# Optimization experiments

Measured on AMD Instinct MI355X. Metric: run time of the kernel, lower is better.

## Reference

```python
import jax, jax.numpy as jnp
import numpy as np

B, C, S, H = 64, 64, 128, 512   # batch, num_centroid, max_seq_length, hidden_size
D = S * H
EPS = 1e-8


def setup_inputs() -> dict:
    key = jax.random.key(0)
    k1, k2 = jax.random.split(key)
    return {
        "input": jax.random.normal(k1, (B, D), dtype=jnp.float32),
        "centroid_weight": jax.random.normal(k2, (C, D), dtype=jnp.float32),
    }


def _gram(x):
    # x: (..., S, H) -> (..., S, S)
    return jnp.einsum('...sh,...th->...st', x, x)


def _centering(g):
    # H @ g @ H with H = I - 11^T/n  ==  g - rowmean - colmean + grandmean
    rm = jnp.mean(g, axis=-1, keepdims=True)
    cm = jnp.mean(g, axis=-2, keepdims=True)
    gm = jnp.mean(g, axis=(-1, -2), keepdims=True)
    return g - rm - cm + gm


def reference(input, centroid_weight):
    # torch.cdist(input, centroid_weight), p=2
    x2 = jnp.sum(input * input, axis=1, keepdims=True)        # (B,1)
    w2 = jnp.sum(centroid_weight * centroid_weight, axis=1)   # (C,)
    d2 = x2 + w2[None, :] - 2.0 * (input @ centroid_weight.T)
    dist = jnp.sqrt(jnp.maximum(d2, 0.0))                     # (B,C)

    xb = input.reshape(B, S, H)
    cw = centroid_weight.reshape(C, S, H)

    cgx = _centering(_gram(xb))   # (B,S,S)
    cgy = _centering(_gram(cw))   # (C,S,S)

    # linear HSIC(x,y) summed over last two dims, broadcast (B,1)x(C) -> (B,C)
    hxy = jnp.einsum('bst,cst->bc', cgx, cgy)
    hxx = jnp.sum(cgx * cgx, axis=(-1, -2))   # (B,)
    hyy = jnp.sum(cgy * cgy, axis=(-1, -2))   # (C,)
    cka_mat = -jnp.log(
        jnp.abs(hxy / (jnp.sqrt(hxx)[:, None] * jnp.sqrt(hyy)[None, :])) + EPS
    )  # (B,C)

    idx = jnp.argmax(cka_mat, axis=-1)                 # (B,)
    sel = centroid_weight[idx].reshape(B, S, H)        # selected centroids
    cgs = _centering(_gram(sel))                       # (B,S,S)

    # second CKA: x is (B,1,S,S), y is (B,S,S) -> broadcast to (B,B) as in torch
    hxy2 = jnp.einsum('bst,cst->bc', cgx, cgs)         # (B,B)
    hyy2 = jnp.sum(cgs * cgs, axis=(-1, -2))           # (B,)
    ratio = jnp.abs(hxy2 / (jnp.sqrt(hxx)[:, None] * jnp.sqrt(hyy2)[None, :]))
    cka_loss = -jnp.log(jnp.mean(ratio) + EPS)         # scalar

    return (cka_loss, dist, centroid_weight, idx)
```

## Files before the change

kernel.cpp:

```cpp
#include <hip/hip_runtime.h>
#include <math.h>

#define Bn 64
#define Cn 64
#define Sn 128
#define Hn 512
#define Dn 65536
#define SSn 16384

using f32x4 = __attribute__((ext_vector_type(4))) float;
using bf16x8 = __attribute__((ext_vector_type(8))) short;
using u16x8 = __attribute__((ext_vector_type(8))) unsigned short;

__device__ __forceinline__ float wredf(float v) {
#pragma unroll
    for (int o = 32; o > 0; o >>= 1) v += __shfl_down(v, o, 64);
    return v;
}

__device__ __forceinline__ unsigned short f2bf(float f) {
    unsigned int u = __float_as_uint(f);
    u += 0x7fffu + ((u >> 16) & 1u);
    return (unsigned short)(u >> 16);
}
__device__ __forceinline__ float bf2f(unsigned short h) {
    return __uint_as_float(((unsigned int)h) << 16);
}

__global__ __launch_bounds__(256) void kA(const float* __restrict__ x,
                                          const float* __restrict__ w,
                                          unsigned short* __restrict__ ghi,
                                          unsigned short* __restrict__ glo,
                                          float* __restrict__ rsT,
                                          float* __restrict__ hpartG,
                                          float* __restrict__ x2,
                                          float* __restrict__ w2,
                                          float* __restrict__ partials,
                                          float* __restrict__ outcpy) {
    __shared__ __align__(16) unsigned char smem[36864];
    const int bid = blockIdx.x;
    const int tid = threadIdx.x;
    if (bid >= 512) {
        const int cid = bid - 512;
        const float4* wsrc = (const float4*)w;
#pragma unroll 4
        for (int p = 0; p < 32; ++p) {
            const size_t f4i = (size_t)cid * 8192 + tid + 256 * p;
            float4 v = wsrc[f4i];
            float* dst = outcpy + 4 * f4i;
            dst[0] = v.x; dst[1] = v.y; dst[2] = v.z; dst[3] = v.w;
        }
        return;
    }
    const int lane = tid & 63;
    const int wv = tid >> 6;
    const int lrow = lane & 15;
    const int lk8 = (lane >> 4) * 8;
    const int crow4 = (lane >> 4) * 4;
    if ((bid & 1) == 0) {
        __shared__ float sredG[4], sredT[4];
        const int gid = bid >> 1;
        const int mat = gid >> 1, half = gid & 1, r0 = half * 64;
        const float* src = (mat < Bn) ? (x + (size_t)mat * Dn) : (w + (size_t)(mat - Bn) * Dn);
        unsigned short* dhi = ghi + (size_t)mat * SSn;
        unsigned short* dlo = glo + (size_t)mat * SSn;
        unsigned short (*hi)[72] = (unsigned short(*)[72])smem;
        unsigned short (*lo)[72] = (unsigned short(*)[72])(smem + 18432);
        f32x4 acc[8] = {};
        float ssq = 0.f;
        float4 cur[8], nxt[8];
#pragma unroll
        for (int p = 0; p < 8; ++p) {
            const int f = tid + 256 * p;
            cur[p] = *(const float4*)(src + (size_t)(f >> 4) * Hn + (f & 15) * 4);
        }
        for (int c = 0; c < 8; ++c) {
#pragma unroll
            for (int p = 0; p < 8; ++p) {
                const int f = tid + 256 * p;
                const int r = f >> 4, c4 = (f & 15) * 4;
                float4 v = cur[p];
                ssq += v.x * v.x + v.y * v.y + v.z * v.z + v.w * v.w;
                unsigned short h0 = f2bf(v.x), h1 = f2bf(v.y), h2 = f2bf(v.z), h3 = f2bf(v.w);
                *(ushort4*)&hi[r][c4] = make_ushort4(h0, h1, h2, h3);
                *(ushort4*)&lo[r][c4] = make_ushort4(f2bf(v.x - bf2f(h0)), f2bf(v.y - bf2f(h1)),
                                                     f2bf(v.z - bf2f(h2)), f2bf(v.w - bf2f(h3)));
            }
            if (c < 7) {
#pragma unroll
                for (int p = 0; p < 8; ++p) {
                    const int f = tid + 256 * p;
                    nxt[p] = *(const float4*)(src + (size_t)(f >> 4) * Hn + (c + 1) * 64 + (f & 15) * 4);
                }
            }
            __syncthreads();
#pragma unroll
            for (int ks = 0; ks < 64; ks += 32) {
                const int arow = r0 + wv * 16 + lrow;
                bf16x8 ah = *(const bf16x8*)&hi[arow][ks + lk8];
                bf16x8 al = *(const bf16x8*)&lo[arow][ks + lk8];
#pragma unroll
                for (int j = 0; j < 8; ++j) {
                    const int brow = j * 16 + lrow;
                    bf16x8 bh = *(const bf16x8*)&hi[brow][ks + lk8];
                    bf16x8 bl = *(const bf16x8*)&lo[brow][ks + lk8];
                    acc[j] = __builtin_amdgcn_mfma_f32_16x16x32_bf16(ah, bh, acc[j], 0, 0, 0);
                    acc[j] = __builtin_amdgcn_mfma_f32_16x16x32_bf16(ah, bl, acc[j], 0, 0, 0);
                    acc[j] = __builtin_amdgcn_mfma_f32_16x16x32_bf16(al, bh, acc[j], 0, 0, 0);
                }
            }
            __syncthreads();
#pragma unroll
            for (int p = 0; p < 8; ++p) cur[p] = nxt[p];
        }
        float sq = 0.f;
#pragma unroll
        for (int j = 0; j < 8; ++j)
#pragma unroll
            for (int r = 0; r < 4; ++r) {
                const float v = acc[j][r];
                sq += v * v;
                const size_t o = (size_t)(r0 + wv * 16 + crow4 + r) * Sn + j * 16 + lrow;
                unsigned short h = f2bf(v);
                dhi[o] = h;
                dlo[o] = f2bf(v - bf2f(h));
            }
#pragma unroll
        for (int r = 0; r < 4; ++r) {
            float rs = 0.f;
#pragma unroll
            for (int j = 0; j < 8; ++j) rs += acc[j][r];
            rs += __shfl_xor(rs, 1, 64);
            rs += __shfl_xor(rs, 2, 64);
            rs += __shfl_xor(rs, 4, 64);
            rs += __shfl_xor(rs, 8, 64);
            if (lrow == 0) rsT[(size_t)(r0 + wv * 16 + crow4 + r) * 128 + mat] = rs;
        }
        sq = wredf(sq);
        ssq = wredf(ssq);
        if (lane == 0) { sredG[wv] = sq; sredT[wv] = ssq; }
        __syncthreads();
        if (tid == 0) {
            hpartG[gid] = sredG[0] + sredG[1] + sredG[2] + sredG[3];
            if (half == 0) {
                float t = sredT[0] + sredT[1] + sredT[2] + sredT[3];
                if (mat < Bn) x2[mat] = t; else w2[mat - Bn] = t;
            }
        }
    } else {
        const int did = bid >> 1;
        unsigned short (*la)[136] = (unsigned short(*)[136])smem;
        unsigned short (*lb)[136] = (unsigned short(*)[136])(smem + 17408);
        f32x4 acc[4] = {};
        for (int c = 0; c < 2; ++c) {
            const int k0 = did * 256 + c * 128;
            __syncthreads();
#pragma unroll
            for (int p = 0; p < 8; ++p) {
                const int f = tid + 256 * p;
                const int row = f >> 5, c4 = (f & 31) * 4;
                float4 vx = *(const float4*)(x + (size_t)row * Dn + k0 + c4);
                float4 vw = *(const float4*)(w + (size_t)row * Dn + k0 + c4);
                *(ushort4*)&la[row][c4] = make_ushort4(f2bf(vx.x), f2bf(vx.y), f2bf(vx.z), f2bf(vx.w));
                *(ushort4*)&lb[row][c4] = make_ushort4(f2bf(vw.x), f2bf(vw.y), f2bf(vw.z), f2bf(vw.w));
            }
            __syncthreads();
#pragma unroll
            for (int ks = 0; ks < 4; ++ks) {
                bf16x8 a = *(const bf16x8*)&la[wv * 16 + lrow][ks * 32 + lk8];
#pragma unroll
                for (int j = 0; j < 4; ++j) {
                    bf16x8 b = *(const bf16x8*)&lb[j * 16 + lrow][ks * 32 + lk8];
                    acc[j] = __builtin_amdgcn_mfma_f32_16x16x32_bf16(a, b, acc[j], 0, 0, 0);
                }
            }
        }
        float* p = partials + (size_t)did * 4096;
#pragma unroll
        for (int j = 0; j < 4; ++j)
#pragma unroll
            for (int r = 0; r < 4; ++r)
                p[(wv * 16 + crow4 + r) * 64 + j * 16 + lrow] = acc[j][r];
    }
}

__global__ __launch_bounds__(256) void kB(const unsigned short* __restrict__ ghi,
                                          const unsigned short* __restrict__ glo,
                                          const float* __restrict__ partials,
                                          const float* __restrict__ rsT,
                                          const float* __restrict__ hpartG,
                                          const float* __restrict__ x2,
                                          const float* __restrict__ w2,
                                          float* __restrict__ partials2,
                                          float* __restrict__ Sv,
                                          float* __restrict__ hxx,
                                          float* __restrict__ hyy,
                                          float* __restrict__ od) {
    __shared__ __align__(16) unsigned char smem[36864];
    const int bid = blockIdx.x;
    const int tid = threadIdx.x;
    if (bid < 256) {
        unsigned short (*lah)[72] = (unsigned short(*)[72])smem;
        unsigned short (*lal)[72] = (unsigned short(*)[72])(smem + 9216);
        unsigned short (*lbh)[72] = (unsigned short(*)[72])(smem + 18432);
        unsigned short (*lbl)[72] = (unsigned short(*)[72])(smem + 27648);
        const int k0 = bid * 64;
#pragma unroll
        for (int i = 0; i < 2; ++i) {
            const int idx = tid + 256 * i;
            const int mat = idx >> 3, c8 = (idx & 7) * 8;
            *(u16x8*)&lah[mat][c8] = *(const u16x8*)(ghi + (size_t)mat * SSn + k0 + c8);
            *(u16x8*)&lal[mat][c8] = *(const u16x8*)(glo + (size_t)mat * SSn + k0 + c8);
            *(u16x8*)&lbh[mat][c8] = *(const u16x8*)(ghi + (size_t)(64 + mat) * SSn + k0 + c8);
            *(u16x8*)&lbl[mat][c8] = *(const u16x8*)(glo + (size_t)(64 + mat) * SSn + k0 + c8);
        }
        __syncthreads();
        const int lane = tid & 63;
        const int wv = tid >> 6;
        const int lrow = lane & 15;
        const int lk8 = (lane >> 4) * 8;
        const int crow4 = (lane >> 4) * 4;
        f32x4 acc[4] = {};
#pragma unroll
        for (int ks = 0; ks < 64; ks += 32) {
            bf16x8 ah = *(const bf16x8*)&lah[wv * 16 + lrow][ks + lk8];
            bf16x8 al = *(const bf16x8*)&lal[wv * 16 + lrow][ks + lk8];
#pragma unroll
            for (int j = 0; j < 4; ++j) {
                bf16x8 bh = *(const bf16x8*)&lbh[j * 16 + lrow][ks + lk8];
                bf16x8 bl = *(const bf16x8*)&lbl[j * 16 + lrow][ks + lk8];
                acc[j] = __builtin_amdgcn_mfma_f32_16x16x32_bf16(ah, bh, acc[j], 0, 0, 0);
                acc[j] = __builtin_amdgcn_mfma_f32_16x16x32_bf16(ah, bl, acc[j], 0, 0, 0);
                acc[j] = __builtin_amdgcn_mfma_f32_16x16x32_bf16(al, bh, acc[j], 0, 0, 0);
            }
        }
        float* p = partials2 + (size_t)bid * 4096;
#pragma unroll
        for (int j = 0; j < 4; ++j)
#pragma unroll
            for (int r = 0; r < 4; ++r)
                p[(wv * 16 + crow4 + r) * 64 + j * 16 + lrow] = acc[j][r];
    } else if (bid < 320) {
        double* red = (double*)smem;
        const int b2 = bid - 256;
        const int o = tid & 63, sl = tid >> 6;
        const int i = b2 * 64 + o;
        double s0 = 0, s1 = 0;
        for (int t = 0; t < 64; t += 2) {
            s0 += (double)partials[(size_t)(sl + 4 * t) * 4096 + i];
            s1 += (double)partials[(size_t)(sl + 4 * (t + 1)) * 4096 + i];
        }
        red[sl * 64 + o] = s0 + s1;
        __syncthreads();
        if (tid < 64) {
            double t = red[tid] + red[64 + tid] + red[128 + tid] + red[192 + tid];
            float d2 = x2[b2] + w2[tid] - 2.f * (float)t;
            od[b2 * 64 + tid] = sqrtf(fmaxf(d2, 0.f));
        }
    } else {
        const int m = tid;
        if (m < 128) {
            float s = 0.f, q = 0.f;
            for (int t = 0; t < 128; ++t) {
                float v = rsT[t * 128 + m];
                s += v; q += v * v;
            }
            Sv[m] = s;
            double val = (double)hpartG[2 * m] + (double)hpartG[2 * m + 1]
                       - (double)q * (1.0 / 64.0) + (double)s * (double)s * (1.0 / 16384.0);
            if (m < 64) hxx[m] = (float)val; else hyy[m - 64] = (float)val;
        }
    }
}

__global__ __launch_bounds__(256) void kC(const float* __restrict__ partials2,
                                          const float* __restrict__ rsT,
                                          const float* __restrict__ Sv,
                                          double* __restrict__ hxy) {
    __shared__ double red[256];
    const int b = blockIdx.x;
    const int o = threadIdx.x & 63;
    const int sl = threadIdx.x >> 6;
    const int i = b * 64 + o;
    double s0 = 0, s1 = 0;
    for (int t = 0; t < 64; t += 2) {
        s0 += (double)partials2[(size_t)(sl + 4 * t) * 4096 + i];
        s1 += (double)partials2[(size_t)(sl + 4 * (t + 1)) * 4096 + i];
    }
    double corr = 0;
    for (int t = 0; t < 32; ++t) {
        const int ss = sl * 32 + t;
        corr += (double)rsT[ss * 128 + b] * (double)rsT[ss * 128 + 64 + o];
    }
    red[sl * 64 + o] = (s0 + s1) - corr * (1.0 / 64.0);
    __syncthreads();
    if (threadIdx.x < 64) {
        double t = red[threadIdx.x] + red[64 + threadIdx.x] +
                   red[128 + threadIdx.x] + red[192 + threadIdx.x];
        t += (double)Sv[b] * (double)Sv[64 + threadIdx.x] * (1.0 / 16384.0);
        hxy[b * 64 + threadIdx.x] = t;
    }
}

__global__ void finalize_k(const double* __restrict__ hxy, const float* __restrict__ hxx,
                           const float* __restrict__ hyy, float* __restrict__ out0,
                           float* __restrict__ oidx) {
    __shared__ double inv_sx[64], inv_sy[64];
    __shared__ int sidx[64];
    __shared__ double sred[4];
    const int tid = threadIdx.x;
    if (tid < 64) {
        inv_sx[tid] = 1.0 / sqrt((double)hxx[tid]);
        inv_sy[tid] = 1.0 / sqrt((double)hyy[tid]);
    }
    __syncthreads();
    if (tid < 64) {
        const int b = tid;
        double best = 1e300; int bi = 0;
        for (int c = 0; c < Cn; ++c) {
            double v = fabs(hxy[b * Cn + c]) * inv_sy[c];
            if (v < best) { best = v; bi = c; }
        }
        sidx[b] = bi;
        oidx[b] = (float)bi;
    }
    __syncthreads();
    double s = 0.0;
    for (int e = tid; e < 4096; e += 256) {
        const int b = e >> 6, c = e & 63;
        const int ic = sidx[c];
        s += fabs(hxy[b * Cn + ic]) * inv_sx[b] * inv_sy[ic];
    }
#pragma unroll
    for (int o = 32; o > 0; o >>= 1) s += __shfl_down(s, o, 64);
    if ((tid & 63) == 0) sred[tid >> 6] = s;
    __syncthreads();
    if (tid == 0) {
        double t = sred[0] + sred[1] + sred[2] + sred[3];
        out0[0] = (float)(-log(t / 4096.0 + 1e-8));
    }
}

extern "C" void kernel_launch(void* const* d_in, const int* in_sizes, int n_in,
                              void* d_out, int out_size, void* d_ws, size_t ws_size,
                              hipStream_t stream) {
    const float* x = (const float*)d_in[0];
    const float* w = (const float*)d_in[1];
    float* out = (float*)d_out;
    float* ws = (float*)d_ws;
    unsigned short* ghi = (unsigned short*)ws;
    unsigned short* glo = (unsigned short*)(ws + 1048576);
    float* partials  = ws + 2097152;
    float* partials2 = ws + 3145728;
    float* rsT    = ws + 4194304;
    float* hpartG = ws + 4210688;
    float* Sv     = ws + 4210944;
    float* x2     = ws + 4211072;
    float* w2     = ws + 4211136;
    float* hxx    = ws + 4211200;
    float* hyy    = ws + 4211264;
    double* hxyD  = (double*)(ws + 4211328);

    kA<<<640, 256, 0, stream>>>(x, w, ghi, glo, rsT, hpartG, x2, w2, partials, out + 4097);
    kB<<<321, 256, 0, stream>>>(ghi, glo, partials, rsT, hpartG, x2, w2,
                                partials2, Sv, hxx, hyy, out + 1);
    kC<<<64, 256, 0, stream>>>(partials2, rsT, Sv, hxyD);
    finalize_k<<<1, 256, 0, stream>>>(hxyD, hxx, hyy, out, out + 4198401);
}
```

Baseline: 120.4 us.

## Compute full Gram per block, store fp32 Grams, use scalar FMA for HSIC

Result: faster. 113.0 us (-6.1%).

```diff
diff --git a/kernel.cpp b/kernel.cpp
--- a/kernel.cpp
+++ b/kernel.cpp
@@ -10,7 +10,6 @@
 
 using f32x4 = __attribute__((ext_vector_type(4))) float;
 using bf16x8 = __attribute__((ext_vector_type(8))) short;
-using u16x8 = __attribute__((ext_vector_type(8))) unsigned short;
 
 __device__ __forceinline__ float wredf(float v) {
 #pragma unroll
@@ -27,25 +26,24 @@
     return __uint_as_float(((unsigned int)h) << 16);
 }
 
-__global__ __launch_bounds__(256) void kA(const float* __restrict__ x,
+__global__ __launch_bounds__(512) void kA(const float* __restrict__ x,
                                           const float* __restrict__ w,
-                                          unsigned short* __restrict__ ghi,
-                                          unsigned short* __restrict__ glo,
+                                          float* __restrict__ gF,
                                           float* __restrict__ rsT,
                                           float* __restrict__ hpartG,
                                           float* __restrict__ x2,
                                           float* __restrict__ w2,
                                           float* __restrict__ partials,
                                           float* __restrict__ outcpy) {
-    __shared__ __align__(16) unsigned char smem[36864];
+    __shared__ __align__(16) unsigned char smem[67584];
     const int bid = blockIdx.x;
     const int tid = threadIdx.x;
-    if (bid >= 512) {
-        const int cid = bid - 512;
+    if (bid >= 256) {
+        const int cid = bid - 256;
         const float4* wsrc = (const float4*)w;
 #pragma unroll 4
         for (int p = 0; p < 32; ++p) {
-            const size_t f4i = (size_t)cid * 8192 + tid + 256 * p;
+            const size_t f4i = (size_t)cid * 16384 + tid + 512 * p;
             float4 v = wsrc[f4i];
             float* dst = outcpy + 4 * f4i;
             dst[0] = v.x; dst[1] = v.y; dst[2] = v.z; dst[3] = v.w;
@@ -57,27 +55,24 @@
     const int lrow = lane & 15;
     const int lk8 = (lane >> 4) * 8;
     const int crow4 = (lane >> 4) * 4;
-    if ((bid & 1) == 0) {
-        __shared__ float sredG[4], sredT[4];
-        const int gid = bid >> 1;
-        const int mat = gid >> 1, half = gid & 1, r0 = half * 64;
+    if (bid < 128) {
+        __shared__ float sA[8], sB[8];
+        const int mat = bid;
         const float* src = (mat < Bn) ? (x + (size_t)mat * Dn) : (w + (size_t)(mat - Bn) * Dn);
-        unsigned short* dhi = ghi + (size_t)mat * SSn;
-        unsigned short* dlo = glo + (size_t)mat * SSn;
         unsigned short (*hi)[72] = (unsigned short(*)[72])smem;
         unsigned short (*lo)[72] = (unsigned short(*)[72])(smem + 18432);
         f32x4 acc[8] = {};
         float ssq = 0.f;
-        float4 cur[8], nxt[8];
-#pragma unroll
-        for (int p = 0; p < 8; ++p) {
-            const int f = tid + 256 * p;
+        float4 cur[4], nxt[4];
+#pragma unroll
+        for (int p = 0; p < 4; ++p) {
+            const int f = tid + 512 * p;
             cur[p] = *(const float4*)(src + (size_t)(f >> 4) * Hn + (f & 15) * 4);
         }
         for (int c = 0; c < 8; ++c) {
 #pragma unroll
-            for (int p = 0; p < 8; ++p) {
-                const int f = tid + 256 * p;
+            for (int p = 0; p < 4; ++p) {
+                const int f = tid + 512 * p;
                 const int r = f >> 4, c4 = (f & 15) * 4;
                 float4 v = cur[p];
                 ssq += v.x * v.x + v.y * v.y + v.z * v.z + v.w * v.w;
@@ -88,15 +83,15 @@
             }
             if (c < 7) {
 #pragma unroll
-                for (int p = 0; p < 8; ++p) {
-                    const int f = tid + 256 * p;
+                for (int p = 0; p < 4; ++p) {
+                    const int f = tid + 512 * p;
                     nxt[p] = *(const float4*)(src + (size_t)(f >> 4) * Hn + (c + 1) * 64 + (f & 15) * 4);
                 }
             }
             __syncthreads();
 #pragma unroll
             for (int ks = 0; ks < 64; ks += 32) {
-                const int arow = r0 + wv * 16 + lrow;
+                const int arow = wv * 16 + lrow;
                 bf16x8 ah = *(const bf16x8*)&hi[arow][ks + lk8];
                 bf16x8 al = *(const bf16x8*)&lo[arow][ks + lk8];
 #pragma unroll
@@ -110,21 +105,19 @@
                 }
             }
             __syncthreads();
-#pragma unroll
-            for (int p = 0; p < 8; ++p) cur[p] = nxt[p];
-        }
+            if (c < 7) {
+#pragma unroll
+                for (int p = 0; p < 4; ++p) cur[p] = nxt[p];
+            }
+        }
+        float* dst = gF + (size_t)mat * SSn + wv * 2048;
         float sq = 0.f;
 #pragma unroll
-        for (int j = 0; j < 8; ++j)
-#pragma unroll
-            for (int r = 0; r < 4; ++r) {
-                const float v = acc[j][r];
-                sq += v * v;
-                const size_t o = (size_t)(r0 + wv * 16 + crow4 + r) * Sn + j * 16 + lrow;
-                unsigned short h = f2bf(v);
-                dhi[o] = h;
-                dlo[o] = f2bf(v - bf2f(h));
-            }
+        for (int j = 0; j < 8; ++j) {
+            f32x4 v = acc[j];
+            sq += v[0] * v[0] + v[1] * v[1] + v[2] * v[2] + v[3] * v[3];
+            *(f32x4*)(dst + j * 256 + lane * 4) = v;
+        }
 #pragma unroll
         for (int r = 0; r < 4; ++r) {
             float rs = 0.f;
@@ -134,31 +127,32 @@
             rs += __shfl_xor(rs, 2, 64);
             rs += __shfl_xor(rs, 4, 64);
             rs += __shfl_xor(rs, 8, 64);
-            if (lrow == 0) rsT[(size_t)(r0 + wv * 16 + crow4 + r) * 128 + mat] = rs;
+            if (lrow == 0) rsT[(size_t)(wv * 16 + crow4 + r) * 128 + mat] = rs;
         }
         sq = wredf(sq);
         ssq = wredf(ssq);
-        if (lane == 0) { sredG[wv] = sq; sredT[wv] = ssq; }
+        if (lane == 0) { sA[wv] = sq; sB[wv] = ssq; }
         __syncthreads();
         if (tid == 0) {
-            hpartG[gid] = sredG[0] + sredG[1] + sredG[2] + sredG[3];
-            if (half == 0) {
-                float t = sredT[0] + sredT[1] + sredT[2] + sredT[3];
-                if (mat < Bn) x2[mat] = t; else w2[mat - Bn] = t;
-            }
+            float g2 = 0.f, tr = 0.f;
+#pragma unroll
+            for (int i = 0; i < 8; ++i) { g2 += sA[i]; tr += sB[i]; }
+            hpartG[mat] = g2;
+            if (mat < Bn) x2[mat] = tr; else w2[mat - Bn] = tr;
         }
     } else {
-        const int did = bid >> 1;
-        unsigned short (*la)[136] = (unsigned short(*)[136])smem;
-        unsigned short (*lb)[136] = (unsigned short(*)[136])(smem + 17408);
-        f32x4 acc[4] = {};
-        for (int c = 0; c < 2; ++c) {
-            const int k0 = did * 256 + c * 128;
+        const int did = bid - 128;
+        unsigned short (*la)[264] = (unsigned short(*)[264])smem;
+        unsigned short (*lb)[264] = (unsigned short(*)[264])(smem + 33792);
+        const int rg = wv >> 1, cgb = (wv & 1) * 2;
+        f32x4 acc[2] = {};
+        for (int cc = 0; cc < 2; ++cc) {
+            const int k0 = did * 512 + cc * 256;
             __syncthreads();
 #pragma unroll
             for (int p = 0; p < 8; ++p) {
-                const int f = tid + 256 * p;
-                const int row = f >> 5, c4 = (f & 31) * 4;
+                const int f = tid + 512 * p;
+                const int row = f >> 6, c4 = (f & 63) * 4;
                 float4 vx = *(const float4*)(x + (size_t)row * Dn + k0 + c4);
                 float4 vw = *(const float4*)(w + (size_t)row * Dn + k0 + c4);
                 *(ushort4*)&la[row][c4] = make_ushort4(f2bf(vx.x), f2bf(vx.y), f2bf(vx.z), f2bf(vx.w));
@@ -166,26 +160,25 @@
             }
             __syncthreads();
 #pragma unroll
-            for (int ks = 0; ks < 4; ++ks) {
-                bf16x8 a = *(const bf16x8*)&la[wv * 16 + lrow][ks * 32 + lk8];
-#pragma unroll
-                for (int j = 0; j < 4; ++j) {
-                    bf16x8 b = *(const bf16x8*)&lb[j * 16 + lrow][ks * 32 + lk8];
-                    acc[j] = __builtin_amdgcn_mfma_f32_16x16x32_bf16(a, b, acc[j], 0, 0, 0);
+            for (int ks = 0; ks < 8; ++ks) {
+                bf16x8 a = *(const bf16x8*)&la[rg * 16 + lrow][ks * 32 + lk8];
+#pragma unroll
+                for (int q = 0; q < 2; ++q) {
+                    bf16x8 b = *(const bf16x8*)&lb[(cgb + q) * 16 + lrow][ks * 32 + lk8];
+                    acc[q] = __builtin_amdgcn_mfma_f32_16x16x32_bf16(a, b, acc[q], 0, 0, 0);
                 }
             }
         }
         float* p = partials + (size_t)did * 4096;
 #pragma unroll
-        for (int j = 0; j < 4; ++j)
+        for (int q = 0; q < 2; ++q)
 #pragma unroll
             for (int r = 0; r < 4; ++r)
-                p[(wv * 16 + crow4 + r) * 64 + j * 16 + lrow] = acc[j][r];
-    }
-}
-
-__global__ __launch_bounds__(256) void kB(const unsigned short* __restrict__ ghi,
-                                          const unsigned short* __restrict__ glo,
+                p[(rg * 16 + crow4 + r) * 64 + (cgb + q) * 16 + lrow] = acc[q][r];
+    }
+}
+
+__global__ __launch_bounds__(256) void kB(const float* __restrict__ gF,
                                           const float* __restrict__ partials,
                                           const float* __restrict__ rsT,
                                           const float* __restrict__ hpartG,
@@ -196,61 +189,49 @@
                                           float* __restrict__ hxx,
                                           float* __restrict__ hyy,
                                           float* __restrict__ od) {
-    __shared__ __align__(16) unsigned char smem[36864];
+    __shared__ __align__(16) unsigned char smem[65536];
     const int bid = blockIdx.x;
     const int tid = threadIdx.x;
     if (bid < 256) {
-        unsigned short (*lah)[72] = (unsigned short(*)[72])smem;
-        unsigned short (*lal)[72] = (unsigned short(*)[72])(smem + 9216);
-        unsigned short (*lbh)[72] = (unsigned short(*)[72])(smem + 18432);
-        unsigned short (*lbl)[72] = (unsigned short(*)[72])(smem + 27648);
+        float (*la)[68] = (float(*)[68])smem;
+        float (*lb)[68] = (float(*)[68])(smem + 17408);
         const int k0 = bid * 64;
-#pragma unroll
-        for (int i = 0; i < 2; ++i) {
-            const int idx = tid + 256 * i;
-            const int mat = idx >> 3, c8 = (idx & 7) * 8;
-            *(u16x8*)&lah[mat][c8] = *(const u16x8*)(ghi + (size_t)mat * SSn + k0 + c8);
-            *(u16x8*)&lal[mat][c8] = *(const u16x8*)(glo + (size_t)mat * SSn + k0 + c8);
-            *(u16x8*)&lbh[mat][c8] = *(const u16x8*)(ghi + (size_t)(64 + mat) * SSn + k0 + c8);
-            *(u16x8*)&lbl[mat][c8] = *(const u16x8*)(glo + (size_t)(64 + mat) * SSn + k0 + c8);
+        const int slc = (tid & 15) * 4;
+        for (int r = tid >> 4; r < 64; r += 16) {
+            *(float4*)&la[r][slc] = *(const float4*)(gF + (size_t)r * SSn + k0 + slc);
+            *(float4*)&lb[r][slc] = *(const float4*)(gF + (size_t)(64 + r) * SSn + k0 + slc);
         }
         __syncthreads();
-        const int lane = tid & 63;
-        const int wv = tid >> 6;
-        const int lrow = lane & 15;
-        const int lk8 = (lane >> 4) * 8;
-        const int crow4 = (lane >> 4) * 4;
-        f32x4 acc[4] = {};
-#pragma unroll
-        for (int ks = 0; ks < 64; ks += 32) {
-            bf16x8 ah = *(const bf16x8*)&lah[wv * 16 + lrow][ks + lk8];
-            bf16x8 al = *(const bf16x8*)&lal[wv * 16 + lrow][ks + lk8];
-#pragma unroll
-            for (int j = 0; j < 4; ++j) {
-                bf16x8 bh = *(const bf16x8*)&lbh[j * 16 + lrow][ks + lk8];
-                bf16x8 bl = *(const bf16x8*)&lbl[j * 16 + lrow][ks + lk8];
-                acc[j] = __builtin_amdgcn_mfma_f32_16x16x32_bf16(ah, bh, acc[j], 0, 0, 0);
-                acc[j] = __builtin_amdgcn_mfma_f32_16x16x32_bf16(ah, bl, acc[j], 0, 0, 0);
-                acc[j] = __builtin_amdgcn_mfma_f32_16x16x32_bf16(al, bh, acc[j], 0, 0, 0);
-            }
+        const int ry = tid >> 4, tx = tid & 15;
+        float acc[4][4] = {};
+        for (int k = 0; k < 64; k += 4) {
+            float4 av[4], bv[4];
+#pragma unroll
+            for (int i = 0; i < 4; ++i) av[i] = *(const float4*)&la[4 * ry + i][k];
+#pragma unroll
+            for (int j = 0; j < 4; ++j) bv[j] = *(const float4*)&lb[16 * j + tx][k];
+#pragma unroll
+            for (int i = 0; i < 4; ++i)
+#pragma unroll
+                for (int j = 0; j < 4; ++j)
+                    acc[i][j] += av[i].x * bv[j].x + av[i].y * bv[j].y +
+                                 av[i].z * bv[j].z + av[i].w * bv[j].w;
         }
         float* p = partials2 + (size_t)bid * 4096;
 #pragma unroll
-        for (int j = 0; j < 4; ++j)
-#pragma unroll
-            for (int r = 0; r < 4; ++r)
-                p[(wv * 16 + crow4 + r) * 64 + j * 16 + lrow] = acc[j][r];
+        for (int i = 0; i < 4; ++i)
+#pragma unroll
+            for (int j = 0; j < 4; ++j)
+                p[(4 * ry + i) * 64 + 16 * j + tx] = acc[i][j];
     } else if (bid < 320) {
         double* red = (double*)smem;
         const int b2 = bid - 256;
         const int o = tid & 63, sl = tid >> 6;
         const int i = b2 * 64 + o;
-        double s0 = 0, s1 = 0;
-        for (int t = 0; t < 64; t += 2) {
-            s0 += (double)partials[(size_t)(sl + 4 * t) * 4096 + i];
-            s1 += (double)partials[(size_t)(sl + 4 * (t + 1)) * 4096 + i];
-        }
-        red[sl * 64 + o] = s0 + s1;
+        double s = 0;
+        for (int t = 0; t < 32; ++t)
+            s += (double)partials[(size_t)(sl + 4 * t) * 4096 + i];
+        red[sl * 64 + o] = s;
         __syncthreads();
         if (tid < 64) {
             double t = red[tid] + red[64 + tid] + red[128 + tid] + red[192 + tid];
@@ -258,17 +239,22 @@
             od[b2 * 64 + tid] = sqrtf(fmaxf(d2, 0.f));
         }
     } else {
-        const int m = tid;
-        if (m < 128) {
+        float* rl = (float*)smem;
+        for (int p = 0; p < 16; ++p) {
+            const int f4 = tid + 256 * p;
+            *(float4*)(rl + 4 * f4) = *(const float4*)(rsT + 4 * f4);
+        }
+        __syncthreads();
+        if (tid < 128) {
             float s = 0.f, q = 0.f;
             for (int t = 0; t < 128; ++t) {
-                float v = rsT[t * 128 + m];
+                float v = rl[t * 128 + tid];
                 s += v; q += v * v;
             }
-            Sv[m] = s;
-            double val = (double)hpartG[2 * m] + (double)hpartG[2 * m + 1]
-                       - (double)q * (1.0 / 64.0) + (double)s * (double)s * (1.0 / 16384.0);
-            if (m < 64) hxx[m] = (float)val; else hyy[m - 64] = (float)val;
+            Sv[tid] = s;
+            double val = (double)hpartG[tid] - (double)q * (1.0 / 64.0)
+                       + (double)s * (double)s * (1.0 / 16384.0);
+            if (tid < 64) hxx[tid] = (float)val; else hyy[tid - 64] = (float)val;
         }
     }
 }
@@ -306,6 +292,8 @@
                            const float* __restrict__ hyy, float* __restrict__ out0,
                            float* __restrict__ oidx) {
     __shared__ double inv_sx[64], inv_sy[64];
+    __shared__ double qv[256];
+    __shared__ int qi[256];
     __shared__ int sidx[64];
     __shared__ double sred[4];
     const int tid = threadIdx.x;
@@ -314,22 +302,30 @@
         inv_sy[tid] = 1.0 / sqrt((double)hyy[tid]);
     }
     __syncthreads();
+    {
+        const int b = tid >> 2, q = tid & 3;
+        double best = 1e300; int bi = 64;
+        for (int c = q * 16; c < q * 16 + 16; ++c) {
+            double v = fabs(hxy[b * 64 + c]) * inv_sy[c];
+            if (v < best) { best = v; bi = c; }
+        }
+        qv[tid] = best; qi[tid] = bi;
+    }
+    __syncthreads();
     if (tid < 64) {
-        const int b = tid;
-        double best = 1e300; int bi = 0;
-        for (int c = 0; c < Cn; ++c) {
-            double v = fabs(hxy[b * Cn + c]) * inv_sy[c];
-            if (v < best) { best = v; bi = c; }
-        }
-        sidx[b] = bi;
-        oidx[b] = (float)bi;
+        double best = qv[4 * tid]; int bi = qi[4 * tid];
+        for (int q = 1; q < 4; ++q) {
+            if (qv[4 * tid + q] < best) { best = qv[4 * tid + q]; bi = qi[4 * tid + q]; }
+        }
+        sidx[tid] = bi;
+        oidx[tid] = (float)bi;
     }
     __syncthreads();
     double s = 0.0;
     for (int e = tid; e < 4096; e += 256) {
         const int b = e >> 6, c = e & 63;
         const int ic = sidx[c];
-        s += fabs(hxy[b * Cn + ic]) * inv_sx[b] * inv_sy[ic];
+        s += fabs(hxy[b * 64 + ic]) * inv_sx[b] * inv_sy[ic];
     }
 #pragma unroll
     for (int o = 32; o > 0; o >>= 1) s += __shfl_down(s, o, 64);
@@ -348,21 +344,20 @@
     const float* w = (const float*)d_in[1];
     float* out = (float*)d_out;
     float* ws = (float*)d_ws;
-    unsigned short* ghi = (unsigned short*)ws;
-    unsigned short* glo = (unsigned short*)(ws + 1048576);
+    float* gF        = ws;
     float* partials  = ws + 2097152;
-    float* partials2 = ws + 3145728;
-    float* rsT    = ws + 4194304;
-    float* hpartG = ws + 4210688;
-    float* Sv     = ws + 4210944;
-    float* x2     = ws + 4211072;
-    float* w2     = ws + 4211136;
-    float* hxx    = ws + 4211200;
-    float* hyy    = ws + 4211264;
-    double* hxyD  = (double*)(ws + 4211328);
-
-    kA<<<640, 256, 0, stream>>>(x, w, ghi, glo, rsT, hpartG, x2, w2, partials, out + 4097);
-    kB<<<321, 256, 0, stream>>>(ghi, glo, partials, rsT, hpartG, x2, w2,
+    float* partials2 = ws + 2621440;
+    float* rsT       = ws + 3670016;
+    float* hpartG    = ws + 3686400;
+    float* Sv        = ws + 3686528;
+    float* x2        = ws + 3686656;
+    float* w2        = ws + 3686720;
+    float* hxx       = ws + 3686784;
+    float* hyy       = ws + 3686848;
+    double* hxyD     = (double*)(ws + 3686912);
+
+    kA<<<320, 512, 0, stream>>>(x, w, gF, rsT, hpartG, x2, w2, partials, out + 4097);
+    kB<<<321, 256, 0, stream>>>(gF, partials, rsT, hpartG, x2, w2,
                                 partials2, Sv, hxx, hyy, out + 1);
     kC<<<64, 256, 0, stream>>>(partials2, rsT, Sv, hxyD);
     finalize_k<<<1, 256, 0, stream>>>(hxyD, hxx, hyy, out, out + 4198401);
```
